# Kernel tuning notes

Measured on AMD Instinct MI355X. Metric: run time of the kernel, lower is better.

Reference implementation:

```python
import jax, jax.numpy as jnp
import numpy as np

B, D_IN, H, D_OUT = 1024, 512, 512, 512


def _act(v):
    # torch.relu(x) ** 2
    r = jnp.maximum(v, 0.0)
    return r * r


def setup_inputs() -> dict:
    key = jax.random.key(0)
    ks = jax.random.split(key, 8)
    x = jax.random.normal(ks[0], (B, D_IN), dtype=jnp.float32)
    # input_to_hidden: Linear(D_IN, H)
    W_in = jax.random.normal(ks[1], (D_IN, H), dtype=jnp.float32) / np.sqrt(D_IN)
    b_in = jax.random.normal(ks[2], (H,), dtype=jnp.float32) * 0.01
    # hidden_to_hidden[i]: Linear(1, H-i-1). Pack into padded arrays [H-1, H]
    # where row i, column j is the weight feeding output index j (valid only j > i).
    W_hh = jax.random.normal(ks[3], (H - 1, H), dtype=jnp.float32) * 0.02
    b_hh = jax.random.normal(ks[4], (H - 1, H), dtype=jnp.float32) * 0.01
    # hidden_to_output: Linear(H, D_OUT)
    W_out = jax.random.normal(ks[5], (H, D_OUT), dtype=jnp.float32) / np.sqrt(H)
    b_out = jax.random.normal(ks[6], (D_OUT,), dtype=jnp.float32) * 0.01
    return {"x": x, "W_in": W_in, "b_in": b_in, "W_hh": W_hh, "b_hh": b_hh,
            "W_out": W_out, "b_out": b_out}


def reference(x, W_in, b_in, W_hh, b_hh, W_out, b_out):
    h0 = _act(x @ W_in + b_in)  # [B, H]
    hid = h0.shape[1]
    col = jnp.arange(hid)

    def step(h, inp):
        i, w, b = inp  # w, b: [H] padded rows
        src = jnp.take(h, i, axis=1)  # [B], uses UPDATED h (strict sequential dep)
        contrib = _act(src[:, None] * w[None, :] + b[None, :])  # [B, H]
        mask = (col > i).astype(h.dtype)  # only columns i+1.. get updated
        return h + contrib * mask[None, :], None

    xs = (jnp.arange(hid - 1), W_hh, b_hh)
    h, _ = jax.lax.scan(step, h0, xs)
    return h @ W_out + b_out  # [B, D_OUT]
```

## Files before the change

### kernel.cpp

```cpp
#include <hip/hip_runtime.h>

#define B_SZ 1024
#define DIN 512
#define HH 512
#define DOUT 512

__global__ __launch_bounds__(256)
void prep_kernel(const float* __restrict__ W_hh,
                 const float* __restrict__ b_hh,
                 float2* __restrict__ wb) {
    int idx = blockIdx.x * 256 + threadIdx.x;
    int i = idx >> 9;
    int j = idx & 511;
    float2 o;
    if (j > i) { o.x = W_hh[idx]; o.y = b_hh[idx]; }
    else       { o.x = 0.0f;      o.y = -1.0f;     }
    wb[idx] = o;
}

template <bool ACT>
__global__ __launch_bounds__(256)
void gemm_kernel(const float* __restrict__ A,
                 const float* __restrict__ Bm,
                 const float* __restrict__ bias,
                 float* __restrict__ C,
                 int M, int N, int K) {
    __shared__ float As[32][34];
    __shared__ float Bs[32][64];

    const int tid = threadIdx.x;
    const int bm = blockIdx.x * 32;
    const int bn = blockIdx.y * 64;
    const int tx = tid & 15;
    const int ty = tid >> 4;
    const int ar = tid >> 3;
    const int ak = (tid & 7) * 4;
    const int bk = tid >> 4;
    const int bc = (tid & 15) * 4;

    float4 av, bv0, bv1;

    auto stage = [&](int kt) {
        av  = *(const float4*)&A[(size_t)(bm + ar) * K + kt + ak];
        bv0 = *(const float4*)&Bm[(size_t)(kt + bk) * N + bn + bc];
        bv1 = *(const float4*)&Bm[(size_t)(kt + bk + 16) * N + bn + bc];
    };

    float acc[2][4] = {{0.f,0.f,0.f,0.f},{0.f,0.f,0.f,0.f}};

    stage(0);
    for (int kt = 0; kt < K; kt += 32) {
        __syncthreads();
        As[ak + 0][ar] = av.x;
        As[ak + 1][ar] = av.y;
        As[ak + 2][ar] = av.z;
        As[ak + 3][ar] = av.w;
        *(float4*)&Bs[bk][bc]      = bv0;
        *(float4*)&Bs[bk + 16][bc] = bv1;
        __syncthreads();
        if (kt + 32 < K) stage(kt + 32);
        __builtin_amdgcn_sched_barrier(0);

        #pragma unroll
        for (int k = 0; k < 32; ++k) {
            const float2 a  = *(const float2*)&As[k][ty * 2];
            const float4 b4 = *(const float4*)&Bs[k][tx * 4];
            acc[0][0] = fmaf(a.x, b4.x, acc[0][0]);
            acc[0][1] = fmaf(a.x, b4.y, acc[0][1]);
            acc[0][2] = fmaf(a.x, b4.z, acc[0][2]);
            acc[0][3] = fmaf(a.x, b4.w, acc[0][3]);
            acc[1][0] = fmaf(a.y, b4.x, acc[1][0]);
            acc[1][1] = fmaf(a.y, b4.y, acc[1][1]);
            acc[1][2] = fmaf(a.y, b4.z, acc[1][2]);
            acc[1][3] = fmaf(a.y, b4.w, acc[1][3]);
        }
    }

    #pragma unroll
    for (int r = 0; r < 2; ++r) {
        const int row = bm + ty * 2 + r;
        const int col = bn + tx * 4;
        float4 v;
        v.x = acc[r][0] + bias[col + 0];
        v.y = acc[r][1] + bias[col + 1];
        v.z = acc[r][2] + bias[col + 2];
        v.w = acc[r][3] + bias[col + 3];
        if (ACT) {
            v.x = fmaxf(v.x, 0.f); v.x *= v.x;
            v.y = fmaxf(v.y, 0.f); v.y *= v.y;
            v.z = fmaxf(v.z, 0.f); v.z *= v.z;
            v.w = fmaxf(v.w, 0.f); v.w *= v.w;
        }
        *(float4*)&C[(size_t)row * N + col] = v;
    }
}

template <int C>
__device__ __forceinline__ void scan_chunk(const float2* __restrict__ wb,
                                           float2* __restrict__ smem,
                                           float hr[8], int lane) {
    constexpr int W2 = 64 * (8 - C);
    constexpr int T  = (C < 4) ? 8 : (C < 6 ? 16 : (C == 6 ? 32 : 64));
    constexpr int NTILES = 64 / T;
    constexpr int NLD = (T * W2) / 256;
    const int tid = threadIdx.x;

    float2 R[16];

    auto stage = [&](int i0) {
        #pragma unroll
        for (int q = 0; q < NLD; ++q) {
            const int e = tid + 256 * q;
            const int r = e / W2;
            const int col = e - r * W2;
            int row = i0 + r;
            if (row > 510) row = 510;
            R[q] = wb[(size_t)row * HH + 64 * C + col];
        }
    };

    stage(64 * C);
    for (int t = 0; t < NTILES; ++t) {
        __syncthreads();
        #pragma unroll
        for (int q = 0; q < NLD; ++q) smem[tid + 256 * q] = R[q];
        __syncthreads();
        if (t + 1 < NTILES) stage(64 * C + (t + 1) * T);
        __builtin_amdgcn_sched_barrier(0);

        #pragma unroll 4
        for (int r = 0; r < T; ++r) {
            const int ii = t * T + r;
            if (C == 7 && ii == 63) break;
            const float hi = __uint_as_float(
                __builtin_amdgcn_readlane(__float_as_uint(hr[C]), ii));
            #pragma unroll
            for (int k = C; k < 8; ++k) {
                const float2 wv = smem[r * W2 + lane + 64 * (k - C)];
                const float tv = fmaf(hi, wv.x, wv.y);
                const float rv = fmaxf(tv, 0.f);
                hr[k] = fmaf(rv, rv, hr[k]);
            }
        }
    }
}

__global__ __launch_bounds__(256)
void scan_kernel(const float2* __restrict__ wb, float* __restrict__ h) {
    __shared__ float2 smem[4096];
    const int lane = threadIdx.x & 63;
    const int wave = threadIdx.x >> 6;
    const int row  = blockIdx.x * 4 + wave;
    float* hrow = h + (size_t)row * HH;

    float hr[8];
    #pragma unroll
    for (int k = 0; k < 8; ++k) hr[k] = hrow[lane + 64 * k];

    scan_chunk<0>(wb, smem, hr, lane);
    scan_chunk<1>(wb, smem, hr, lane);
    scan_chunk<2>(wb, smem, hr, lane);
    scan_chunk<3>(wb, smem, hr, lane);
    scan_chunk<4>(wb, smem, hr, lane);
    scan_chunk<5>(wb, smem, hr, lane);
    scan_chunk<6>(wb, smem, hr, lane);
    scan_chunk<7>(wb, smem, hr, lane);

    #pragma unroll
    for (int k = 0; k < 8; ++k) hrow[lane + 64 * k] = hr[k];
}

extern "C" void kernel_launch(void* const* d_in, const int* in_sizes, int n_in,
                              void* d_out, int out_size, void* d_ws, size_t ws_size,
                              hipStream_t stream) {
    const float* x     = (const float*)d_in[0];
    const float* W_in  = (const float*)d_in[1];
    const float* b_in  = (const float*)d_in[2];
    const float* W_hh  = (const float*)d_in[3];
    const float* b_hh  = (const float*)d_in[4];
    const float* W_out = (const float*)d_in[5];
    const float* b_out = (const float*)d_in[6];
    float* out = (float*)d_out;

    float2* wb = (float2*)d_ws;
    float*  h  = (float*)((char*)d_ws + (1u << 21));

    prep_kernel<<<dim3(1022), dim3(256), 0, stream>>>(W_hh, b_hh, wb);

    gemm_kernel<true><<<dim3(B_SZ / 32, HH / 64), dim3(256), 0, stream>>>(
        x, W_in, b_in, h, B_SZ, HH, DIN);

    scan_kernel<<<dim3(256), dim3(256), 0, stream>>>(wb, h);

    gemm_kernel<false><<<dim3(B_SZ / 32, DOUT / 64), dim3(256), 0, stream>>>(
        h, W_out, b_out, out, B_SZ, DOUT, HH);
}
```

Measured before the change: 166.0 us.

## Replace fp32 SIMT GEMMs with split-bf16 MFMA GEMMs using pre-packed fragments

Both dense GEMMs now run on bf16 MFMA 16x16x32 instructions. Each fp32 operand is split into high and low bf16 parts and three cross terms are accumulated, so accuracy stays close to fp32. Inputs are converted into fragment-ordered layouts in a merged prep kernel, plus an extra conversion pass over the hidden state after the scan. This trades more launches and conversion traffic for much higher matrix throughput, while the sequential scan stays unchanged.

New measurement: 158.5 us. 4.5% less time.

```diff
diff --git a/kernel.cpp b/kernel.cpp
--- a/kernel.cpp
+++ b/kernel.cpp
@@ -5,93 +5,174 @@
 #define HH 512
 #define DOUT 512
 
-__global__ __launch_bounds__(256)
-void prep_kernel(const float* __restrict__ W_hh,
-                 const float* __restrict__ b_hh,
-                 float2* __restrict__ wb) {
-    int idx = blockIdx.x * 256 + threadIdx.x;
-    int i = idx >> 9;
-    int j = idx & 511;
-    float2 o;
-    if (j > i) { o.x = W_hh[idx]; o.y = b_hh[idx]; }
-    else       { o.x = 0.0f;      o.y = -1.0f;     }
-    wb[idx] = o;
+typedef short bf16x8 __attribute__((ext_vector_type(8)));
+typedef float f32x4 __attribute__((ext_vector_type(4)));
+
+__device__ __forceinline__ unsigned short f2bf(float f) {
+    unsigned int u = __float_as_uint(f);
+    u += 0x7FFFu + ((u >> 16) & 1u);
+    return (unsigned short)(u >> 16);
+}
+__device__ __forceinline__ float bf2f(unsigned short s) {
+    return __uint_as_float(((unsigned int)s) << 16);
+}
+
+__device__ __forceinline__ void conv_split_body(const float* __restrict__ src,
+                                                uint4* __restrict__ dst, int t) {
+    const int lane = t & 63;
+    const int fb   = t >> 6;
+    const int ks   = fb >> 6;
+    const int mf   = fb & 63;
+    const int row  = mf * 16 + (lane & 15);
+    const int kb   = ks * 32 + ((lane >> 4) << 3);
+    const int term = kb >> 9;
+    const int c    = kb & 511;
+    const float4 a0 = *(const float4*)&src[(size_t)row * 512 + c];
+    const float4 a1 = *(const float4*)&src[(size_t)row * 512 + c + 4];
+    const float av[8] = {a0.x, a0.y, a0.z, a0.w, a1.x, a1.y, a1.z, a1.w};
+    unsigned short o[8];
+    #pragma unroll
+    for (int j = 0; j < 8; ++j) {
+        unsigned short hi = f2bf(av[j]);
+        o[j] = (term == 1) ? f2bf(av[j] - bf2f(hi)) : hi;
+    }
+    uint4 v;
+    v.x = (unsigned int)o[0] | ((unsigned int)o[1] << 16);
+    v.y = (unsigned int)o[2] | ((unsigned int)o[3] << 16);
+    v.z = (unsigned int)o[4] | ((unsigned int)o[5] << 16);
+    v.w = (unsigned int)o[6] | ((unsigned int)o[7] << 16);
+    dst[t] = v;
+}
+
+__device__ __forceinline__ void convW_body(const float* __restrict__ W,
+                                           uint4* __restrict__ dst, int t) {
+    const int lane = t & 63;
+    const int fb   = t >> 6;
+    const int ks   = fb >> 5;
+    const int nf   = fb & 31;
+    const int col  = nf * 16 + (lane & 15);
+    const int kb   = ks * 32 + ((lane >> 4) << 3);
+    const int term = kb >> 9;
+    const int c0   = kb & 511;
+    unsigned short o[8];
+    #pragma unroll
+    for (int j = 0; j < 8; ++j) {
+        const float f = W[(size_t)(c0 + j) * 512 + col];
+        unsigned short hi = f2bf(f);
+        o[j] = (term == 2) ? f2bf(f - bf2f(hi)) : hi;
+    }
+    uint4 v;
+    v.x = (unsigned int)o[0] | ((unsigned int)o[1] << 16);
+    v.y = (unsigned int)o[2] | ((unsigned int)o[3] << 16);
+    v.z = (unsigned int)o[4] | ((unsigned int)o[5] << 16);
+    v.w = (unsigned int)o[6] | ((unsigned int)o[7] << 16);
+    dst[t] = v;
+}
+
+__global__ __launch_bounds__(256)
+void prep_all(const float* __restrict__ W_hh, const float* __restrict__ b_hh,
+              float2* __restrict__ wb,
+              const float* __restrict__ x, uint4* __restrict__ Afr,
+              const float* __restrict__ W_in, uint4* __restrict__ Bin,
+              const float* __restrict__ W_out, uint4* __restrict__ Bout) {
+    const int b = blockIdx.x;
+    const int tid = threadIdx.x;
+    if (b < 1022) {
+        const int idx = b * 256 + tid;
+        const int i = idx >> 9;
+        const int j = idx & 511;
+        float2 o;
+        if (j > i) { o.x = W_hh[idx]; o.y = b_hh[idx]; }
+        else       { o.x = 0.0f;      o.y = -1.0f;     }
+        wb[idx] = o;
+    } else if (b < 1790) {
+        conv_split_body(x, Afr, (b - 1022) * 256 + tid);
+    } else if (b < 2174) {
+        convW_body(W_in, Bin, (b - 1790) * 256 + tid);
+    } else {
+        convW_body(W_out, Bout, (b - 2174) * 256 + tid);
+    }
+}
+
+__global__ __launch_bounds__(256)
+void conv_h(const float* __restrict__ h, uint4* __restrict__ Afr) {
+    conv_split_body(h, Afr, blockIdx.x * 256 + threadIdx.x);
 }
 
 template <bool ACT>
 __global__ __launch_bounds__(256)
-void gemm_kernel(const float* __restrict__ A,
-                 const float* __restrict__ Bm,
-                 const float* __restrict__ bias,
-                 float* __restrict__ C,
-                 int M, int N, int K) {
-    __shared__ float As[32][34];
-    __shared__ float Bs[32][64];
-
-    const int tid = threadIdx.x;
-    const int bm = blockIdx.x * 32;
-    const int bn = blockIdx.y * 64;
-    const int tx = tid & 15;
-    const int ty = tid >> 4;
-    const int ar = tid >> 3;
-    const int ak = (tid & 7) * 4;
-    const int bk = tid >> 4;
-    const int bc = (tid & 15) * 4;
-
-    float4 av, bv0, bv1;
-
-    auto stage = [&](int kt) {
-        av  = *(const float4*)&A[(size_t)(bm + ar) * K + kt + ak];
-        bv0 = *(const float4*)&Bm[(size_t)(kt + bk) * N + bn + bc];
-        bv1 = *(const float4*)&Bm[(size_t)(kt + bk + 16) * N + bn + bc];
+void mfma_gemm(const uint4* __restrict__ Ag,
+               const uint4* __restrict__ Bg,
+               const float* __restrict__ bias,
+               float* __restrict__ C) {
+    __shared__ uint4 lds[2][768];
+    const int tid  = threadIdx.x;
+    const int lane = tid & 63;
+    const int w    = tid >> 6;
+    const int wr   = w & 1;
+    const int wc   = w >> 1;
+    const int mf0  = blockIdx.x * 4;
+    const int nf0  = blockIdx.y * 2;
+
+    const int a_mfs = (tid >> 6) & 3;
+    const int b_ks  = tid >> 7;
+    const int b_nfs = (tid >> 6) & 1;
+
+    uint4 R0, R1, R2;
+    auto stage = [&](int s) {
+        const int ks0 = s * 2;
+        R0 = Ag[(size_t)((ks0    ) * 64 + mf0 + a_mfs) * 64 + lane];
+        R1 = Ag[(size_t)((ks0 + 1) * 64 + mf0 + a_mfs) * 64 + lane];
+        R2 = Bg[(size_t)((ks0 + b_ks) * 32 + nf0 + b_nfs) * 64 + lane];
     };
 
-    float acc[2][4] = {{0.f,0.f,0.f,0.f},{0.f,0.f,0.f,0.f}};
+    f32x4 acc0 = {0.f, 0.f, 0.f, 0.f};
+    f32x4 acc1 = {0.f, 0.f, 0.f, 0.f};
 
     stage(0);
-    for (int kt = 0; kt < K; kt += 32) {
+    lds[0][tid] = R0; lds[0][256 + tid] = R1; lds[0][512 + tid] = R2;
+    stage(1);
+    __syncthreads();
+
+    for (int s = 0; s < 24; ++s) {
+        const int cur = s & 1;
+        if (s + 1 < 24) {
+            const int nxt = cur ^ 1;
+            lds[nxt][tid] = R0; lds[nxt][256 + tid] = R1; lds[nxt][512 + tid] = R2;
+        }
+        if (s + 2 < 24) stage(s + 2);
+        __builtin_amdgcn_sched_barrier(0);
+
+        bf16x8 aF[2][2], bF[2];
+        #pragma unroll
+        for (int ksL = 0; ksL < 2; ++ksL) {
+            #pragma unroll
+            for (int mfL = 0; mfL < 2; ++mfL)
+                aF[ksL][mfL] = *(const bf16x8*)&lds[cur][ksL * 256 + (wr * 2 + mfL) * 64 + lane];
+            bF[ksL] = *(const bf16x8*)&lds[cur][512 + (ksL * 2 + wc) * 64 + lane];
+        }
+        #pragma unroll
+        for (int ksL = 0; ksL < 2; ++ksL) {
+            acc0 = __builtin_amdgcn_mfma_f32_16x16x32_bf16(aF[ksL][0], bF[ksL], acc0, 0, 0, 0);
+            acc1 = __builtin_amdgcn_mfma_f32_16x16x32_bf16(aF[ksL][1], bF[ksL], acc1, 0, 0, 0);
+        }
         __syncthreads();
-        As[ak + 0][ar] = av.x;
-        As[ak + 1][ar] = av.y;
-        As[ak + 2][ar] = av.z;
-        As[ak + 3][ar] = av.w;
-        *(float4*)&Bs[bk][bc]      = bv0;
-        *(float4*)&Bs[bk + 16][bc] = bv1;
-        __syncthreads();
-        if (kt + 32 < K) stage(kt + 32);
-        __builtin_amdgcn_sched_barrier(0);
-
-        #pragma unroll
-        for (int k = 0; k < 32; ++k) {
-            const float2 a  = *(const float2*)&As[k][ty * 2];
-            const float4 b4 = *(const float4*)&Bs[k][tx * 4];
-            acc[0][0] = fmaf(a.x, b4.x, acc[0][0]);
-            acc[0][1] = fmaf(a.x, b4.y, acc[0][1]);
-            acc[0][2] = fmaf(a.x, b4.z, acc[0][2]);
-            acc[0][3] = fmaf(a.x, b4.w, acc[0][3]);
-            acc[1][0] = fmaf(a.y, b4.x, acc[1][0]);
-            acc[1][1] = fmaf(a.y, b4.y, acc[1][1]);
-            acc[1][2] = fmaf(a.y, b4.z, acc[1][2]);
-            acc[1][3] = fmaf(a.y, b4.w, acc[1][3]);
-        }
-    }
-
-    #pragma unroll
-    for (int r = 0; r < 2; ++r) {
-        const int row = bm + ty * 2 + r;
-        const int col = bn + tx * 4;
-        float4 v;
-        v.x = acc[r][0] + bias[col + 0];
-        v.y = acc[r][1] + bias[col + 1];
-        v.z = acc[r][2] + bias[col + 2];
-        v.w = acc[r][3] + bias[col + 3];
-        if (ACT) {
-            v.x = fmaxf(v.x, 0.f); v.x *= v.x;
-            v.y = fmaxf(v.y, 0.f); v.y *= v.y;
-            v.z = fmaxf(v.z, 0.f); v.z *= v.z;
-            v.w = fmaxf(v.w, 0.f); v.w *= v.w;
-        }
-        *(float4*)&C[(size_t)row * N + col] = v;
+    }
+
+    const int colg   = (nf0 + wc) * 16 + (lane & 15);
+    const float bv   = bias[colg];
+    const int rbase0 = (mf0 + wr * 2) * 16 + ((lane >> 4) << 2);
+    #pragma unroll
+    for (int r = 0; r < 4; ++r) {
+        float v = acc0[r] + bv;
+        if (ACT) { v = fmaxf(v, 0.f); v = v * v; }
+        C[(size_t)(rbase0 + r) * 512 + colg] = v;
+    }
+    #pragma unroll
+    for (int r = 0; r < 4; ++r) {
+        float v = acc1[r] + bv;
+        if (ACT) { v = fmaxf(v, 0.f); v = v * v; }
+        C[(size_t)(rbase0 + 16 + r) * 512 + colg] = v;
     }
 }
 
@@ -182,16 +263,21 @@
     const float* b_out = (const float*)d_in[6];
     float* out = (float*)d_out;
 
-    float2* wb = (float2*)d_ws;
-    float*  h  = (float*)((char*)d_ws + (1u << 21));
-
-    prep_kernel<<<dim3(1022), dim3(256), 0, stream>>>(W_hh, b_hh, wb);
-
-    gemm_kernel<true><<<dim3(B_SZ / 32, HH / 64), dim3(256), 0, stream>>>(
-        x, W_in, b_in, h, B_SZ, HH, DIN);
+    char* ws = (char*)d_ws;
+    float2* wb  = (float2*)ws;
+    float*  h   = (float*)(ws + 0x200000u);
+    uint4*  Afr = (uint4*)(ws + 0x400000u);
+    uint4*  Bin = (uint4*)(ws + 0x700000u);
+    uint4*  Bout= (uint4*)(ws + 0x880000u);
+
+    prep_all<<<dim3(2558), dim3(256), 0, stream>>>(W_hh, b_hh, wb,
+                                                   x, Afr, W_in, Bin, W_out, Bout);
+
+    mfma_gemm<true><<<dim3(16, 16), dim3(256), 0, stream>>>(Afr, Bin, b_in, h);
 
     scan_kernel<<<dim3(256), dim3(256), 0, stream>>>(wb, h);
 
-    gemm_kernel<false><<<dim3(B_SZ / 32, DOUT / 64), dim3(256), 0, stream>>>(
-        h, W_out, b_out, out, B_SZ, DOUT, HH);
-}
+    conv_h<<<dim3(768), dim3(256), 0, stream>>>(h, Afr);
+
+    mfma_gemm<false><<<dim3(16, 16), dim3(256), 0, stream>>>(Afr, Bout, b_out, out);
+}
```
